# Kernel tuning notes

Measured on AMD Instinct MI355X. Metric: run time of the kernel, lower is better.

Reference implementation:

```python
import jax, jax.numpy as jnp
import numpy as np

N, E, G = 100000, 1600000, 64   # nodes, edges, graphs
IN, H, OUT = 32, 128, 3


def setup_inputs() -> dict:
    key = jax.random.key(0)
    ks = jax.random.split(key, 24)
    def w(k, i, o):
        return (jax.random.normal(k, (i, o), jnp.float32) / np.sqrt(i)).astype(jnp.float32)
    inp = {
        "x": jax.random.normal(ks[0], (N, IN), jnp.float32),
        "edge_index": jax.random.randint(ks[1], (2, E), 0, N, dtype=jnp.int32).astype(jnp.int64),
        "batch": jnp.sort(jax.random.randint(ks[2], (N,), 0, G, dtype=jnp.int32)).astype(jnp.int64),
        # SAGEConv layer 0 (in->hidden): lin_l (neighbors, with bias), lin_r (root, no bias)
        "Wl0": w(ks[3], IN, H), "bl0": jnp.zeros((H,), jnp.float32), "Wr0": w(ks[4], IN, H),
        # SAGEConv layers 1,2 (hidden->hidden)
        "Wl1": w(ks[5], H, H), "bl1": jnp.zeros((H,), jnp.float32), "Wr1": w(ks[6], H, H),
        "Wl2": w(ks[7], H, H), "bl2": jnp.zeros((H,), jnp.float32), "Wr2": w(ks[8], H, H),
        # output head
        "Wfc": w(ks[9], H, OUT), "bfc": jnp.zeros((OUT,), jnp.float32),
        # aux MLP on (dim1, dim3)
        "Wa1": w(ks[10], 2, H), "ba1": jnp.zeros((H,), jnp.float32),
        "Wa2": w(ks[11], H, H), "ba2": jnp.zeros((H,), jnp.float32),
        "Wao": w(ks[12], H, 1), "bao": jnp.zeros((1,), jnp.float32),
    }
    return inp


def _sage_conv(x, src, dst, Wl, bl, Wr):
    # PyG SAGEConv (mean aggr): out = lin_l(mean_{j in N(i)} x_j) + lin_r(x_i)
    msg = x[src]                                   # [E, d] gather
    agg = jax.ops.segment_sum(msg, dst, num_segments=N)
    cnt = jax.ops.segment_sum(jnp.ones((src.shape[0],), x.dtype), dst, num_segments=N)
    mean = agg / jnp.maximum(cnt, 1.0)[:, None]
    return mean @ Wl + bl + x @ Wr


def reference(x, edge_index, batch,
              Wl0, bl0, Wr0, Wl1, bl1, Wr1, Wl2, bl2, Wr2,
              Wfc, bfc, Wa1, ba1, Wa2, ba2, Wao, bao):
    src, dst = edge_index[0], edge_index[1]
    h = jax.nn.relu(_sage_conv(x, src, dst, Wl0, bl0, Wr0))   # dropout is identity in eval
    h = jax.nn.relu(_sage_conv(h, src, dst, Wl1, bl1, Wr1))
    h = jax.nn.relu(_sage_conv(h, src, dst, Wl2, bl2, Wr2))
    main = h @ Wfc + bfc                                      # [N, 3]
    dim1, dim3 = main[:, 0], main[:, 2]
    aux_in = jnp.stack([dim1, dim3], axis=-1)                 # [N, 2]
    a = jax.nn.relu(aux_in @ Wa1 + ba1)
    a = jax.nn.relu(a @ Wa2 + ba2)
    aux_out = (a @ Wao + bao)[:, 0]                           # [N]
    final = jnp.stack([dim1, aux_out, dim3], axis=-1)         # [N, 3]
    # global mean pool over graph ids
    s = jax.ops.segment_sum(final, batch, num_segments=G)
    c = jax.ops.segment_sum(jnp.ones((final.shape[0],), final.dtype), batch, num_segments=G)
    return s / jnp.maximum(c, 1.0)[:, None]                   # [G, 3]
```

## Files before the change

kernel.cpp:

```cpp
#include <hip/hip_runtime.h>

#define NR 128
#define PART_CH 4096
typedef unsigned short ushortT;
typedef __attribute__((ext_vector_type(8))) short short8;
typedef __attribute__((ext_vector_type(4))) float float4v;
typedef __attribute__((ext_vector_type(2))) float float2v;

__device__ __forceinline__ unsigned short f32_to_bf16_rne(float f) {
    unsigned u = __float_as_uint(f);
    unsigned r = (u + 0x7fffu + ((u >> 16) & 1u)) >> 16;
    return (unsigned short)r;
}

__device__ __forceinline__ unsigned char f32_to_fp8(float f) {
    return (unsigned char)(__builtin_amdgcn_cvt_pk_fp8_f32(f, f, 0, false) & 0xff);
}

__device__ __forceinline__ void accum8(float* acc, uint4 v) {
    unsigned u[4] = {v.x, v.y, v.z, v.w};
#pragma unroll
    for (int q = 0; q < 4; q++) {
        acc[2 * q]     += __uint_as_float(u[q] << 16);
        acc[2 * q + 1] += __uint_as_float(u[q] & 0xffff0000u);
    }
}


__launch_bounds__(256)
__global__ void bucket_count(const int* __restrict__ dst, int* __restrict__ bcnt, int E, int NB) {
    __shared__ int h[1024];
    int t = threadIdx.x;
    for (int j = t; j < NB; j += 256) h[j] = 0;
    __syncthreads();
    int e0 = blockIdx.x * PART_CH;
    int e1 = min(e0 + PART_CH, E);
    for (int base = e0; base < e1; base += 2048) {
        int idx = base + t;
        int d[8];
        int cnt = 0;
#pragma unroll
        for (int u = 0; u < 8; u++) {
            int e = idx + u * 256;
            if (e < e1) d[cnt++] = dst[e];
        }
        for (int u = 0; u < cnt; u++) atomicAdd(&h[d[u] >> 7], 1);
    }
    __syncthreads();
    for (int j = t; j < NB; j += 256) {
        int v = h[j];
        if (v) atomicAdd(&bcnt[j], v);
    }
}

__launch_bounds__(256)
__global__ void bucket_scan(const int* __restrict__ bcnt, int* __restrict__ bstart,
                            int* __restrict__ gcur, int NB, int E) {
    __shared__ int sh[256];
    int t = threadIdx.x;
    int v[4];
    int tot = 0;
#pragma unroll
    for (int j = 0; j < 4; j++) {
        int idx = t * 4 + j;
        v[j] = (idx < NB) ? bcnt[idx] : 0;
        tot += v[j];
    }
    sh[t] = tot;
    __syncthreads();
    for (int off = 1; off < 256; off <<= 1) {
        int add = (t >= off) ? sh[t - off] : 0;
        __syncthreads();
        sh[t] += add;
        __syncthreads();
    }
    int run = sh[t] - tot;
#pragma unroll
    for (int j = 0; j < 4; j++) {
        int idx = t * 4 + j;
        if (idx < NB) { bstart[idx] = run; gcur[idx] = run; }
        run += v[j];
    }
    if (t == 0) bstart[NB] = E;
}

__launch_bounds__(256)
__global__ void partition_edges(const int* __restrict__ src, const int* __restrict__ dst,
                                int* __restrict__ gcur, unsigned* __restrict__ packed,
                                int E, int NB) {
    __shared__ int hist[1024];
    __shared__ int base[1024];
    int t = threadIdx.x;
    int e0 = blockIdx.x * PART_CH;
    int e1 = min(e0 + PART_CH, E);
    for (int j = t; j < NB; j += 256) hist[j] = 0;
    __syncthreads();
    for (int bb = e0; bb < e1; bb += 2048) {
        int idx = bb + t;
        int d[8];
        int cnt = 0;
#pragma unroll
        for (int u = 0; u < 8; u++) {
            int e = idx + u * 256;
            if (e < e1) d[cnt++] = dst[e];
        }
        for (int u = 0; u < cnt; u++) atomicAdd(&hist[d[u] >> 7], 1);
    }
    __syncthreads();
    for (int j = t; j < NB; j += 256) {
        int h = hist[j];
        base[j] = h ? atomicAdd(&gcur[j], h) : 0;
    }
    __syncthreads();
    for (int j = t; j < NB; j += 256) hist[j] = base[j];
    __syncthreads();
    for (int bb = e0; bb < e1; bb += 2048) {
        int idx = bb + t;
        int d[8], s[8];
        int cnt = 0;
#pragma unroll
        for (int u = 0; u < 8; u++) {
            int e = idx + u * 256;
            if (e < e1) { d[cnt] = dst[e]; s[cnt] = src[e]; cnt++; }
        }
        for (int u = 0; u < cnt; u++) {
            int dd = d[u];
            int pos = atomicAdd(&hist[dd >> 7], 1);
            packed[pos] = (unsigned)s[u] | ((unsigned)(dd & (NR - 1)) << 17);
        }
    }
}

__launch_bounds__(256)
__global__ void bucket_sort(const unsigned* __restrict__ packed, const int* __restrict__ bstart,
                            int* __restrict__ row_start, int* __restrict__ srcs, int N) {
    __shared__ int cnt[NR];
    __shared__ int sc[NR];
    __shared__ int cur[NR];
    int b = blockIdx.x, t = threadIdx.x;
    int nb0 = b * NR;
    int nnode = min(NR, N - nb0);
    int lo = bstart[b], hi = bstart[b + 1];
    if (t < NR) cnt[t] = 0;
    __syncthreads();
    for (int bb = lo; bb < hi; bb += 2048) {
        int idx = bb + t;
        unsigned pk[8];
        int c = 0;
#pragma unroll
        for (int u = 0; u < 8; u++) {
            int e = idx + u * 256;
            if (e < hi) pk[c++] = packed[e];
        }
        for (int u = 0; u < c; u++) atomicAdd(&cnt[pk[u] >> 17], 1);
    }
    __syncthreads();
    if (t < NR) sc[t] = cnt[t];
    __syncthreads();
    for (int off = 1; off < NR; off <<= 1) {
        int add = (t >= off && t < NR) ? sc[t - off] : 0;
        __syncthreads();
        if (t < NR) sc[t] += add;
        __syncthreads();
    }
    if (t < nnode) {
        int s = lo + sc[t] - cnt[t];
        row_start[nb0 + t] = s;
        cur[t] = s;
    }
    if (t == 0 && nb0 + nnode == N) row_start[N] = hi;
    __syncthreads();
    for (int bb = lo; bb < hi; bb += 2048) {
        int idx = bb + t;
        unsigned pk[8];
        int c = 0;
#pragma unroll
        for (int u = 0; u < 8; u++) {
            int e = idx + u * 256;
            if (e < hi) pk[c++] = packed[e];
        }
        for (int u = 0; u < c; u++) {
            int pos = atomicAdd(&cur[pk[u] >> 17], 1);
            srcs[pos] = (int)(pk[u] & 0x1FFFFu);
        }
    }
}


__global__ void prep_fused(const float* __restrict__ x, ushortT* __restrict__ xbf, int n4,
                           const float* __restrict__ Wl0, const float* __restrict__ Wr0,
                           const float* __restrict__ Wl1, const float* __restrict__ Wr1,
                           const float* __restrict__ Wl2, const float* __restrict__ Wr2,
                           const float* __restrict__ Wa2,
                           ushortT* __restrict__ Wt0, ushortT* __restrict__ Wt1,
                           ushortT* __restrict__ Wt2, ushortT* __restrict__ Wa2t) {
    int tid0 = blockIdx.x * 256 + threadIdx.x;
    if (tid0 < n4) {
        float4 v = ((const float4*)x)[tid0];
        ushort4 o;
        o.x = f32_to_bf16_rne(v.x);
        o.y = f32_to_bf16_rne(v.y);
        o.z = f32_to_bf16_rne(v.z);
        o.w = f32_to_bf16_rne(v.w);
        ((ushort4*)xbf)[tid0] = o;
        return;
    }
    int tid = tid0 - n4;
    if (tid < 8192) {
        int col = tid >> 6, k = tid & 63;
        float v = (k < 32) ? Wl0[k * 128 + col] : Wr0[(k - 32) * 128 + col];
        Wt0[col * 64 + ((k + 8 * col) & 63)] = f32_to_bf16_rne(v);
    } else if (tid < 8192 + 32768) {
        int j = tid - 8192;
        int col = j >> 8, k = j & 255;
        float v = (k < 128) ? Wl1[k * 128 + col] : Wr1[(k - 128) * 128 + col];
        Wt1[col * 256 + ((k + 8 * col) & 255)] = f32_to_bf16_rne(v);
    } else if (tid < 8192 + 65536) {
        int j = tid - 8192 - 32768;
        int col = j >> 8, k = j & 255;
        float v = (k < 128) ? Wl2[k * 128 + col] : Wr2[(k - 128) * 128 + col];
        Wt2[col * 256 + ((k + 8 * col) & 255)] = f32_to_bf16_rne(v);
    } else if (tid < 8192 + 65536 + 16384) {
        int j = tid - 8192 - 65536;
        int col = j >> 7, k = j & 127;
        Wa2t[col * 128 + ((k + 8 * col) & 127)] = f32_to_bf16_rne(Wa2[k * 128 + col]);
    }
}


template <bool FP8, int NKS>
__device__ __forceinline__ void gather_accum(const void* __restrict__ gat, int s, int q, float* ag) {
    if constexpr (FP8) {
        const uint2* hp = (const uint2*)gat;
        size_t base = (size_t)s * 16 + q;
        uint2 c[NKS];
#pragma unroll
        for (int ks = 0; ks < NKS; ks++) c[ks] = hp[base + ks * 4];
#pragma unroll
        for (int ks = 0; ks < NKS; ks++) {
            float2v l0 = __builtin_amdgcn_cvt_pk_f32_fp8(c[ks].x, false);
            float2v h0 = __builtin_amdgcn_cvt_pk_f32_fp8(c[ks].x, true);
            float2v l1 = __builtin_amdgcn_cvt_pk_f32_fp8(c[ks].y, false);
            float2v h1 = __builtin_amdgcn_cvt_pk_f32_fp8(c[ks].y, true);
            ag[ks * 8 + 0] += l0.x; ag[ks * 8 + 1] += l0.y;
            ag[ks * 8 + 2] += h0.x; ag[ks * 8 + 3] += h0.y;
            ag[ks * 8 + 4] += l1.x; ag[ks * 8 + 5] += l1.y;
            ag[ks * 8 + 6] += h1.x; ag[ks * 8 + 7] += h1.y;
        }
    } else {
        const uint4* xp = (const uint4*)gat;
        uint4 v = xp[(size_t)s * 4 + q];
        accum8(ag, v);
    }
}

template <int KH, bool IN_FP8>
__launch_bounds__(256, 2)
__global__ void gemm_agg(const void* __restrict__ gat, const ushortT* __restrict__ Ah,
                         const int* __restrict__ srcs, const int* __restrict__ rs,
                         const ushortT* __restrict__ Wt, const float* __restrict__ bias,
                         ushortT* __restrict__ outbf, unsigned char* __restrict__ outf8, int n) {
    constexpr int KT = 2 * KH;
    constexpr int NKS = KH / 32;
    __shared__ __attribute__((aligned(16))) ushortT sW[128 * KT];
    int t = threadIdx.x;
    constexpr int TOT16 = 128 * KT * 2 / 16;
    {
        const uint4* Wg = (const uint4*)Wt;
        uint4* Ws = (uint4*)sW;
#pragma unroll
        for (int j = 0; j < TOT16 / 256; j++) Ws[t + j * 256] = Wg[t + j * 256];
    }
    int wv = t >> 6, lane = t & 63;
    int q = lane >> 4, cid = lane & 15;
    int rbase = blockIdx.x * 128 + wv * 32;
    int r0 = rbase + cid, r1 = r0 + 16;
    int r0c = min(r0, n - 1), r1c = min(r1, n - 1);

    float ag0[NKS * 8], ag1[NKS * 8];
#pragma unroll
    for (int j = 0; j < NKS * 8; j++) { ag0[j] = 0.f; ag1[j] = 0.f; }
    int lo0 = rs[r0c], n0 = rs[r0c + 1] - lo0;
    int lo1 = rs[r1c], n1 = rs[r1c + 1] - lo1;
    int mx = max(n0, n1);
    for (int i = 0; i < mx; i += 2) {
        bool v00 = i < n0, v01 = (i + 1) < n0;
        bool v10 = i < n1, v11 = (i + 1) < n1;
        int s00 = srcs[v00 ? lo0 + i : 0];
        int s01 = srcs[v01 ? lo0 + i + 1 : 0];
        int s10 = srcs[v10 ? lo1 + i : 0];
        int s11 = srcs[v11 ? lo1 + i + 1 : 0];
        if (v00) gather_accum<IN_FP8, NKS>(gat, s00, q, ag0);
        if (v01) gather_accum<IN_FP8, NKS>(gat, s01, q, ag0);
        if (v10) gather_accum<IN_FP8, NKS>(gat, s10, q, ag1);
        if (v11) gather_accum<IN_FP8, NKS>(gat, s11, q, ag1);
    }
    float inv0 = 1.0f / (float)max(n0, 1);
    float inv1 = 1.0f / (float)max(n1, 1);
    short8 am0[NKS], am1[NKS];
#pragma unroll
    for (int ks = 0; ks < NKS; ks++)
#pragma unroll
        for (int j = 0; j < 8; j++) {
            am0[ks][j] = (short)f32_to_bf16_rne(ag0[ks * 8 + j] * inv0);
            am1[ks][j] = (short)f32_to_bf16_rne(ag1[ks * 8 + j] * inv1);
        }
    __syncthreads();

    float4v acc[2][8];
#pragma unroll
    for (int i = 0; i < 2; i++)
#pragma unroll
        for (int j = 0; j < 8; j++) acc[i][j] = (float4v){0.f, 0.f, 0.f, 0.f};
    int swz = q * 8 + 8 * cid;
#pragma unroll
    for (int ks = 0; ks < KT / 32; ++ks) {
        int kk = ks * 32;
        short8 a0, a1;
        if (ks < NKS) {
            a0 = am0[ks];
            a1 = am1[ks];
        } else {
            int kc = kk - KH;
            a0 = *(const short8*)(Ah + (size_t)r0c * KH + kc + q * 8);
            a1 = *(const short8*)(Ah + (size_t)r1c * KH + kc + q * 8);
        }
#pragma unroll
        for (int j = 0; j < 8; ++j) {
            int col = j * 16 + cid;
            int p = (kk + swz + j * 128) & (KT - 1);
            short8 b = *(const short8*)(sW + col * KT + p);
            acc[0][j] = __builtin_amdgcn_mfma_f32_16x16x32_bf16(a0, b, acc[0][j], 0, 0, 0);
            acc[1][j] = __builtin_amdgcn_mfma_f32_16x16x32_bf16(a1, b, acc[1][j], 0, 0, 0);
        }
    }
    float bo[8];
#pragma unroll
    for (int j = 0; j < 8; ++j) bo[j] = bias[j * 16 + cid];
#pragma unroll
    for (int i = 0; i < 2; ++i) {
#pragma unroll
        for (int rr = 0; rr < 4; ++rr) {
            int row = rbase + i * 16 + q * 4 + rr;
            if (row < n) {
#pragma unroll
                for (int j = 0; j < 8; ++j) {
                    int col = j * 16 + cid;
                    float v = fmaxf(acc[i][j][rr] + bo[j], 0.f);
                    outbf[(size_t)row * 128 + col] = f32_to_bf16_rne(v);
                    outf8[(size_t)row * 128 + col] = f32_to_fp8(v);
                }
            }
        }
    }
}


__launch_bounds__(256, 2)
__global__ void gemm_agg_fin(const void* __restrict__ gat, const ushortT* __restrict__ Ah,
                             const int* __restrict__ srcs, const int* __restrict__ rs,
                             const ushortT* __restrict__ Wt, const float* __restrict__ bias,
                             const float* __restrict__ Wfc, const float* __restrict__ bfc,
                             const ushortT* __restrict__ Wa2t, const float* __restrict__ Wa1,
                             const float* __restrict__ ba1, const float* __restrict__ ba2,
                             const float* __restrict__ Wao, const float* __restrict__ bao,
                             float* __restrict__ fin, int n) {
    constexpr int KH = 128, KT = 256, NKS = 4;
    __shared__ __attribute__((aligned(16))) ushortT sW[128 * KT];
    __shared__ float sD1[128], sD3[128];
    __shared__ float sWa1a[128], sWa1b[128], sBa1[128];
    int t = threadIdx.x;
    {
        const uint4* Wg = (const uint4*)Wt;
        uint4* Ws = (uint4*)sW;
#pragma unroll
        for (int j = 0; j < 16; j++) Ws[t + j * 256] = Wg[t + j * 256];
    }
    if (t < 128) { sWa1a[t] = Wa1[t]; sWa1b[t] = Wa1[128 + t]; sBa1[t] = ba1[t]; }
    int wv = t >> 6, lane = t & 63;
    int q = lane >> 4, cid = lane & 15;
    int blk0 = blockIdx.x * 128;
    int rbase = blk0 + wv * 32;
    int r0 = rbase + cid, r1 = r0 + 16;
    int r0c = min(r0, n - 1), r1c = min(r1, n - 1);

    float ag0[NKS * 8], ag1[NKS * 8];
#pragma unroll
    for (int j = 0; j < NKS * 8; j++) { ag0[j] = 0.f; ag1[j] = 0.f; }
    int lo0 = rs[r0c], n0 = rs[r0c + 1] - lo0;
    int lo1 = rs[r1c], n1 = rs[r1c + 1] - lo1;
    int mx = max(n0, n1);
    for (int i = 0; i < mx; i += 2) {
        bool v00 = i < n0, v01 = (i + 1) < n0;
        bool v10 = i < n1, v11 = (i + 1) < n1;
        int s00 = srcs[v00 ? lo0 + i : 0];
        int s01 = srcs[v01 ? lo0 + i + 1 : 0];
        int s10 = srcs[v10 ? lo1 + i : 0];
        int s11 = srcs[v11 ? lo1 + i + 1 : 0];
        if (v00) gather_accum<true, NKS>(gat, s00, q, ag0);
        if (v01) gather_accum<true, NKS>(gat, s01, q, ag0);
        if (v10) gather_accum<true, NKS>(gat, s10, q, ag1);
        if (v11) gather_accum<true, NKS>(gat, s11, q, ag1);
    }
    float inv0 = 1.0f / (float)max(n0, 1);
    float inv1 = 1.0f / (float)max(n1, 1);
    short8 am0[NKS], am1[NKS];
#pragma unroll
    for (int ks = 0; ks < NKS; ks++)
#pragma unroll
        for (int j = 0; j < 8; j++) {
            am0[ks][j] = (short)f32_to_bf16_rne(ag0[ks * 8 + j] * inv0);
            am1[ks][j] = (short)f32_to_bf16_rne(ag1[ks * 8 + j] * inv1);
        }
    __syncthreads();

    float4v acc[2][8];
#pragma unroll
    for (int i = 0; i < 2; i++)
#pragma unroll
        for (int j = 0; j < 8; j++) acc[i][j] = (float4v){0.f, 0.f, 0.f, 0.f};
    int swz = q * 8 + 8 * cid;
#pragma unroll
    for (int ks = 0; ks < KT / 32; ++ks) {
        int kk = ks * 32;
        short8 a0, a1;
        if (ks < NKS) {
            a0 = am0[ks];
            a1 = am1[ks];
        } else {
            int kc = kk - KH;
            a0 = *(const short8*)(Ah + (size_t)r0c * KH + kc + q * 8);
            a1 = *(const short8*)(Ah + (size_t)r1c * KH + kc + q * 8);
        }
#pragma unroll
        for (int j = 0; j < 8; ++j) {
            int col = j * 16 + cid;
            int p = (kk + swz + j * 128) & (KT - 1);
            short8 b = *(const short8*)(sW + col * KT + p);
            acc[0][j] = __builtin_amdgcn_mfma_f32_16x16x32_bf16(a0, b, acc[0][j], 0, 0, 0);
            acc[1][j] = __builtin_amdgcn_mfma_f32_16x16x32_bf16(a1, b, acc[1][j], 0, 0, 0);
        }
    }

    float bo[8], w1[8], w3[8];
#pragma unroll
    for (int j = 0; j < 8; ++j) {
        int col = j * 16 + cid;
        bo[j] = bias[col];
        w1[j] = Wfc[col * 3 + 0];
        w3[j] = Wfc[col * 3 + 2];
    }
    float bfc0 = bfc[0], bfc2 = bfc[2];
#pragma unroll
    for (int i = 0; i < 2; ++i) {
#pragma unroll
        for (int rr = 0; rr < 4; ++rr) {
            float p1 = 0.f, p3 = 0.f;
#pragma unroll
            for (int j = 0; j < 8; ++j) {
                float v = fmaxf(acc[i][j][rr] + bo[j], 0.f);
                p1 += v * w1[j];
                p3 += v * w3[j];
            }
            p1 += __shfl_xor(p1, 1, 64); p3 += __shfl_xor(p3, 1, 64);
            p1 += __shfl_xor(p1, 2, 64); p3 += __shfl_xor(p3, 2, 64);
            p1 += __shfl_xor(p1, 4, 64); p3 += __shfl_xor(p3, 4, 64);
            p1 += __shfl_xor(p1, 8, 64); p3 += __shfl_xor(p3, 8, 64);
            int rowl = wv * 32 + i * 16 + q * 4 + rr;
            if (cid == 0) {
                float d1 = p1 + bfc0, d3 = p3 + bfc2;
                sD1[rowl] = d1;
                sD3[rowl] = d3;
                int row = blk0 + rowl;
                if (row < n) {
                    fin[(size_t)row * 3 + 0] = d1;
                    fin[(size_t)row * 3 + 2] = d3;
                }
            }
        }
    }
    __syncthreads();

    {
        const uint4* Wg = (const uint4*)Wa2t;
        uint4* Ws = (uint4*)sW;
#pragma unroll
        for (int j = 0; j < 8; j++) Ws[t + j * 256] = Wg[t + j * 256];
    }
    __syncthreads();

    int rl0 = wv * 32 + cid, rl1 = rl0 + 16;
    float d1a = sD1[rl0], d3a = sD3[rl0];
    float d1b = sD1[rl1], d3b = sD3[rl1];
    float4v hacc[2][8];
#pragma unroll
    for (int i = 0; i < 2; i++)
#pragma unroll
        for (int j = 0; j < 8; j++) hacc[i][j] = (float4v){0.f, 0.f, 0.f, 0.f};
#pragma unroll
    for (int ks = 0; ks < 4; ++ks) {
        int k0 = ks * 32 + q * 8;
        short8 a0, a1;
#pragma unroll
        for (int j = 0; j < 8; ++j) {
            int k = k0 + j;
            float w0 = sWa1a[k], w1h = sWa1b[k], bb = sBa1[k];
            float v0 = fmaxf(fmaf(d1a, w0, fmaf(d3a, w1h, bb)), 0.f);
            float v1 = fmaxf(fmaf(d1b, w0, fmaf(d3b, w1h, bb)), 0.f);
            a0[j] = (short)f32_to_bf16_rne(v0);
            a1[j] = (short)f32_to_bf16_rne(v1);
        }
        int p = (ks * 32 + swz) & 127;
#pragma unroll
        for (int j = 0; j < 8; ++j) {
            short8 b = *(const short8*)(sW + (j * 16 + cid) * 128 + p);
            hacc[0][j] = __builtin_amdgcn_mfma_f32_16x16x32_bf16(a0, b, hacc[0][j], 0, 0, 0);
            hacc[1][j] = __builtin_amdgcn_mfma_f32_16x16x32_bf16(a1, b, hacc[1][j], 0, 0, 0);
        }
    }
    float b2[8], wo[8];
#pragma unroll
    for (int j = 0; j < 8; ++j) {
        int col = j * 16 + cid;
        b2[j] = ba2[col];
        wo[j] = Wao[col];
    }
    float bao0 = bao[0];
#pragma unroll
    for (int i = 0; i < 2; ++i) {
#pragma unroll
        for (int rr = 0; rr < 4; ++rr) {
            float s = 0.f;
#pragma unroll
            for (int j = 0; j < 8; ++j) s += fmaxf(hacc[i][j][rr] + b2[j], 0.f) * wo[j];
            s += __shfl_xor(s, 1, 64);
            s += __shfl_xor(s, 2, 64);
            s += __shfl_xor(s, 4, 64);
            s += __shfl_xor(s, 8, 64);
            int row = blk0 + wv * 32 + i * 16 + q * 4 + rr;
            if (cid == 0 && row < n) fin[(size_t)row * 3 + 1] = s + bao0;
        }
    }
}


__global__ void pool_kernel(const float* __restrict__ fin, const int* __restrict__ batch,
                            float* __restrict__ out, int n) {
    int g = blockIdx.x, t = threadIdx.x;
    int lo = 0, hi = n;
    while (lo < hi) { int mid = (lo + hi) >> 1; if (batch[mid] < g) lo = mid + 1; else hi = mid; }
    int start = lo;
    lo = 0; hi = n;
    while (lo < hi) { int mid = (lo + hi) >> 1; if (batch[mid] < g + 1) lo = mid + 1; else hi = mid; }
    int end = lo;
    float s0 = 0.f, s1 = 0.f, s2 = 0.f;
    for (int i = start + t; i < end; i += 256) {
        s0 += fin[(size_t)i * 3 + 0];
        s1 += fin[(size_t)i * 3 + 1];
        s2 += fin[(size_t)i * 3 + 2];
    }
    __shared__ float r0[256], r1[256], r2[256];
    r0[t] = s0; r1[t] = s1; r2[t] = s2;
    __syncthreads();
    for (int off = 128; off > 0; off >>= 1) {
        if (t < off) { r0[t] += r0[t + off]; r1[t] += r1[t + off]; r2[t] += r2[t + off]; }
        __syncthreads();
    }
    if (t == 0) {
        float c = (float)max(end - start, 1);
        out[g * 3 + 0] = r0[0] / c;
        out[g * 3 + 1] = r1[0] / c;
        out[g * 3 + 2] = r2[0] / c;
    }
}


extern "C" void kernel_launch(void* const* d_in, const int* in_sizes, int n_in,
                              void* d_out, int out_size, void* d_ws, size_t ws_size,
                              hipStream_t stream) {
    const float* x    = (const float*)d_in[0];
    const int*   ei   = (const int*)d_in[1];
    const int*   batch= (const int*)d_in[2];
    const float* Wl0  = (const float*)d_in[3];
    const float* bl0  = (const float*)d_in[4];
    const float* Wr0  = (const float*)d_in[5];
    const float* Wl1  = (const float*)d_in[6];
    const float* bl1  = (const float*)d_in[7];
    const float* Wr1  = (const float*)d_in[8];
    const float* Wl2  = (const float*)d_in[9];
    const float* bl2  = (const float*)d_in[10];
    const float* Wr2  = (const float*)d_in[11];
    const float* Wfc  = (const float*)d_in[12];
    const float* bfc  = (const float*)d_in[13];
    const float* Wa1  = (const float*)d_in[14];
    const float* ba1  = (const float*)d_in[15];
    const float* Wa2  = (const float*)d_in[16];
    const float* ba2  = (const float*)d_in[17];
    const float* Wao  = (const float*)d_in[18];
    const float* bao  = (const float*)d_in[19];

    const int N = in_sizes[0] / 32;
    const int E = in_sizes[1] / 2;
    const int G = out_size / 3;
    const int* src = ei;
    const int* dst = ei + E;
    float* out = (float*)d_out;
    const int NB = (N + NR - 1) / NR;

    char* p = (char*)d_ws;
    auto carve = [&](size_t bytes) {
        void* r = (void*)p;
        p += (bytes + 255) & ~(size_t)255;
        return r;
    };
    int*           bcnt     = (int*)carve((size_t)NB * 4);
    int*           bstart   = (int*)carve((size_t)(NB + 1) * 4);
    int*           gcur     = (int*)carve((size_t)NB * 4);
    int*           row_start= (int*)carve((size_t)(N + 1) * 4);
    unsigned*      packed   = (unsigned*)carve((size_t)E * 4);
    int*           srcs     = (int*)carve((size_t)E * 4);
    ushortT*       xbf      = (ushortT*)carve((size_t)N * 32 * 2);
    ushortT*       hbf0     = (ushortT*)carve((size_t)N * 128 * 2);
    ushortT*       hbf1     = (ushortT*)carve((size_t)N * 128 * 2);
    unsigned char* hf8_0    = (unsigned char*)carve((size_t)N * 128);
    unsigned char* hf8_1    = (unsigned char*)carve((size_t)N * 128);
    float*         fin      = (float*)carve((size_t)N * 3 * 4);
    ushortT*       Wt0      = (ushortT*)carve((size_t)128 * 64 * 2);
    ushortT*       Wt1      = (ushortT*)carve((size_t)128 * 256 * 2);
    ushortT*       Wt2      = (ushortT*)carve((size_t)128 * 256 * 2);
    ushortT*       Wa2t     = (ushortT*)carve((size_t)128 * 128 * 2);

    const int gemm_grid = (N + 127) / 128;
    const int part_grid = (E + PART_CH - 1) / PART_CH;
    const int n4 = N * 32 / 4;

    prep_fused<<<(n4 + 90112 + 255) / 256, 256, 0, stream>>>(
        x, xbf, n4, Wl0, Wr0, Wl1, Wr1, Wl2, Wr2, Wa2, Wt0, Wt1, Wt2, Wa2t);

    hipMemsetAsync(bcnt, 0, (size_t)NB * 4, stream);
    bucket_count<<<part_grid, 256, 0, stream>>>(dst, bcnt, E, NB);
    bucket_scan<<<1, 256, 0, stream>>>(bcnt, bstart, gcur, NB, E);
    partition_edges<<<part_grid, 256, 0, stream>>>(src, dst, gcur, packed, E, NB);
    bucket_sort<<<NB, 256, 0, stream>>>(packed, bstart, row_start, srcs, N);

    gemm_agg<32, false><<<gemm_grid, 256, 0, stream>>>(
        (const void*)xbf, xbf, srcs, row_start, Wt0, bl0, hbf0, hf8_0, N);
    gemm_agg<128, true><<<gemm_grid, 256, 0, stream>>>(
        (const void*)hf8_0, hbf0, srcs, row_start, Wt1, bl1, hbf1, hf8_1, N);
    gemm_agg_fin<<<gemm_grid, 256, 0, stream>>>(
        (const void*)hf8_1, hbf1, srcs, row_start, Wt2, bl2, Wfc, bfc,
        Wa2t, Wa1, ba1, ba2, Wao, bao, fin, N);

    pool_kernel<<<G, 256, 0, stream>>>(fin, batch, out, N);
}
```

Baseline: 408.9 us.

## Shrink GEMM-agg tiles to 64 rows, halve LDS weights, batch 8-edge gathers

The fused aggregate+GEMM kernels now handle 16 rows per wave (64 per block) instead of 32. The weight matrix is split into two 128-wide halves loaded into LDS one after the other, which halves the shared-memory footprint, and launch bounds rise from 2 to 4 blocks per CU. The neighbor gather is restructured to prefetch 8 source indices and issue 8 feature loads at once, using 32-byte FP8 loads per lane, with the FP8 output columns permuted to match. The goal is more memory-level parallelism and occupancy for the latency-bound gathers, at the cost of reloading weights per block, an extra sync, and more blocks.

```diff
diff --git a/kernel.cpp b/kernel.cpp
--- a/kernel.cpp
+++ b/kernel.cpp
@@ -23,6 +23,19 @@
     for (int q = 0; q < 4; q++) {
         acc[2 * q]     += __uint_as_float(u[q] << 16);
         acc[2 * q + 1] += __uint_as_float(u[q] & 0xffff0000u);
+    }
+}
+
+__device__ __forceinline__ void accum32_fp8(float* ag, uint4 A, uint4 B) {
+    unsigned w[8] = {A.x, A.y, A.z, A.w, B.x, B.y, B.z, B.w};
+#pragma unroll
+    for (int m = 0; m < 8; m++) {
+        float2v lo = __builtin_amdgcn_cvt_pk_f32_fp8(w[m], false);
+        float2v hi = __builtin_amdgcn_cvt_pk_f32_fp8(w[m], true);
+        ag[4 * m + 0] += lo.x;
+        ag[4 * m + 1] += lo.y;
+        ag[4 * m + 2] += hi.x;
+        ag[4 * m + 3] += hi.y;
     }
 }
 
@@ -214,12 +227,12 @@
         int j = tid - 8192;
         int col = j >> 8, k = j & 255;
         float v = (k < 128) ? Wl1[k * 128 + col] : Wr1[(k - 128) * 128 + col];
-        Wt1[col * 256 + ((k + 8 * col) & 255)] = f32_to_bf16_rne(v);
+        Wt1[(k >> 7) * 16384 + col * 128 + (((k & 127) + 8 * col) & 127)] = f32_to_bf16_rne(v);
     } else if (tid < 8192 + 65536) {
         int j = tid - 8192 - 32768;
         int col = j >> 8, k = j & 255;
         float v = (k < 128) ? Wl2[k * 128 + col] : Wr2[(k - 128) * 128 + col];
-        Wt2[col * 256 + ((k + 8 * col) & 255)] = f32_to_bf16_rne(v);
+        Wt2[(k >> 7) * 16384 + col * 128 + (((k & 127) + 8 * col) & 127)] = f32_to_bf16_rne(v);
     } else if (tid < 8192 + 65536 + 16384) {
         int j = tid - 8192 - 65536;
         int col = j >> 7, k = j & 127;
@@ -228,135 +241,160 @@
 }
 
 
-template <bool FP8, int NKS>
-__device__ __forceinline__ void gather_accum(const void* __restrict__ gat, int s, int q, float* ag) {
-    if constexpr (FP8) {
-        const uint2* hp = (const uint2*)gat;
-        size_t base = (size_t)s * 16 + q;
-        uint2 c[NKS];
-#pragma unroll
-        for (int ks = 0; ks < NKS; ks++) c[ks] = hp[base + ks * 4];
-#pragma unroll
-        for (int ks = 0; ks < NKS; ks++) {
-            float2v l0 = __builtin_amdgcn_cvt_pk_f32_fp8(c[ks].x, false);
-            float2v h0 = __builtin_amdgcn_cvt_pk_f32_fp8(c[ks].x, true);
-            float2v l1 = __builtin_amdgcn_cvt_pk_f32_fp8(c[ks].y, false);
-            float2v h1 = __builtin_amdgcn_cvt_pk_f32_fp8(c[ks].y, true);
-            ag[ks * 8 + 0] += l0.x; ag[ks * 8 + 1] += l0.y;
-            ag[ks * 8 + 2] += h0.x; ag[ks * 8 + 3] += h0.y;
-            ag[ks * 8 + 4] += l1.x; ag[ks * 8 + 5] += l1.y;
-            ag[ks * 8 + 6] += h1.x; ag[ks * 8 + 7] += h1.y;
-        }
-    } else {
-        const uint4* xp = (const uint4*)gat;
-        uint4 v = xp[(size_t)s * 4 + q];
-        accum8(ag, v);
-    }
-}
+__device__ __forceinline__ void gather_fp8(const uint4* __restrict__ hp, const int* __restrict__ srcs,
+                                           int lo, int deg, int q, float* ag) {
+    int nb = (deg + 7) >> 3;
+    if (nb == 0) return;
+    int last = lo + deg - 1;
+    int sA[8];
+#pragma unroll
+    for (int u = 0; u < 8; u++) sA[u] = srcs[min(lo + u, last)];
+    for (int b = 0; b < nb; b++) {
+        uint4 va[8], vb[8];
+#pragma unroll
+        for (int u = 0; u < 8; u++) {
+            size_t bs = (size_t)sA[u] * 8 + q * 2;
+            va[u] = hp[bs];
+            vb[u] = hp[bs + 1];
+        }
+        int e0 = lo + (b + 1) * 8;
+        if (b + 1 < nb) {
+#pragma unroll
+            for (int u = 0; u < 8; u++) sA[u] = srcs[min(e0 + u, last)];
+        }
+        int rem = deg - b * 8;
+#pragma unroll
+        for (int u = 0; u < 8; u++)
+            if (u < rem) accum32_fp8(ag, va[u], vb[u]);
+    }
+}
+
+__device__ __forceinline__ void gather_bf16(const uint4* __restrict__ xp, const int* __restrict__ srcs,
+                                            int lo, int deg, int q, float* ag) {
+    int nb = (deg + 7) >> 3;
+    if (nb == 0) return;
+    int last = lo + deg - 1;
+    int sA[8];
+#pragma unroll
+    for (int u = 0; u < 8; u++) sA[u] = srcs[min(lo + u, last)];
+    for (int b = 0; b < nb; b++) {
+        uint4 va[8];
+#pragma unroll
+        for (int u = 0; u < 8; u++) va[u] = xp[(size_t)sA[u] * 4 + q];
+        int e0 = lo + (b + 1) * 8;
+        if (b + 1 < nb) {
+#pragma unroll
+            for (int u = 0; u < 8; u++) sA[u] = srcs[min(e0 + u, last)];
+        }
+        int rem = deg - b * 8;
+#pragma unroll
+        for (int u = 0; u < 8; u++)
+            if (u < rem) accum8(ag, va[u]);
+    }
+}
+
 
 template <int KH, bool IN_FP8>
-__launch_bounds__(256, 2)
+__launch_bounds__(256, 4)
 __global__ void gemm_agg(const void* __restrict__ gat, const ushortT* __restrict__ Ah,
                          const int* __restrict__ srcs, const int* __restrict__ rs,
                          const ushortT* __restrict__ Wt, const float* __restrict__ bias,
                          ushortT* __restrict__ outbf, unsigned char* __restrict__ outf8, int n) {
-    constexpr int KT = 2 * KH;
     constexpr int NKS = KH / 32;
-    __shared__ __attribute__((aligned(16))) ushortT sW[128 * KT];
+    constexpr int KTH = (KH == 32) ? 64 : 128;
+    __shared__ __attribute__((aligned(16))) ushortT sW[128 * KTH];
     int t = threadIdx.x;
-    constexpr int TOT16 = 128 * KT * 2 / 16;
     {
         const uint4* Wg = (const uint4*)Wt;
         uint4* Ws = (uint4*)sW;
 #pragma unroll
-        for (int j = 0; j < TOT16 / 256; j++) Ws[t + j * 256] = Wg[t + j * 256];
+        for (int j = 0; j < (128 * KTH / 8) / 256; j++) Ws[t + j * 256] = Wg[t + j * 256];
     }
     int wv = t >> 6, lane = t & 63;
     int q = lane >> 4, cid = lane & 15;
-    int rbase = blockIdx.x * 128 + wv * 32;
-    int r0 = rbase + cid, r1 = r0 + 16;
-    int r0c = min(r0, n - 1), r1c = min(r1, n - 1);
-
-    float ag0[NKS * 8], ag1[NKS * 8];
-#pragma unroll
-    for (int j = 0; j < NKS * 8; j++) { ag0[j] = 0.f; ag1[j] = 0.f; }
-    int lo0 = rs[r0c], n0 = rs[r0c + 1] - lo0;
-    int lo1 = rs[r1c], n1 = rs[r1c + 1] - lo1;
-    int mx = max(n0, n1);
-    for (int i = 0; i < mx; i += 2) {
-        bool v00 = i < n0, v01 = (i + 1) < n0;
-        bool v10 = i < n1, v11 = (i + 1) < n1;
-        int s00 = srcs[v00 ? lo0 + i : 0];
-        int s01 = srcs[v01 ? lo0 + i + 1 : 0];
-        int s10 = srcs[v10 ? lo1 + i : 0];
-        int s11 = srcs[v11 ? lo1 + i + 1 : 0];
-        if (v00) gather_accum<IN_FP8, NKS>(gat, s00, q, ag0);
-        if (v01) gather_accum<IN_FP8, NKS>(gat, s01, q, ag0);
-        if (v10) gather_accum<IN_FP8, NKS>(gat, s10, q, ag1);
-        if (v11) gather_accum<IN_FP8, NKS>(gat, s11, q, ag1);
-    }
-    float inv0 = 1.0f / (float)max(n0, 1);
-    float inv1 = 1.0f / (float)max(n1, 1);
-    short8 am0[NKS], am1[NKS];
+    int row = blockIdx.x * 64 + wv * 16 + cid;
+    int rc = min(row, n - 1);
+
+    float ag[NKS * 8];
+#pragma unroll
+    for (int j = 0; j < NKS * 8; j++) ag[j] = 0.f;
+    int lo = rs[rc], deg = rs[rc + 1] - lo;
+    if constexpr (IN_FP8) gather_fp8((const uint4*)gat, srcs, lo, deg, q, ag);
+    else                  gather_bf16((const uint4*)gat, srcs, lo, deg, q, ag);
+    float inv = 1.0f / (float)max(deg, 1);
+    short8 am[NKS];
 #pragma unroll
     for (int ks = 0; ks < NKS; ks++)
 #pragma unroll
-        for (int j = 0; j < 8; j++) {
-            am0[ks][j] = (short)f32_to_bf16_rne(ag0[ks * 8 + j] * inv0);
-            am1[ks][j] = (short)f32_to_bf16_rne(ag1[ks * 8 + j] * inv1);
-        }
-    __syncthreads();
-
-    float4v acc[2][8];
-#pragma unroll
-    for (int i = 0; i < 2; i++)
-#pragma unroll
-        for (int j = 0; j < 8; j++) acc[i][j] = (float4v){0.f, 0.f, 0.f, 0.f};
-    int swz = q * 8 + 8 * cid;
-#pragma unroll
-    for (int ks = 0; ks < KT / 32; ++ks) {
-        int kk = ks * 32;
-        short8 a0, a1;
-        if (ks < NKS) {
-            a0 = am0[ks];
-            a1 = am1[ks];
-        } else {
-            int kc = kk - KH;
-            a0 = *(const short8*)(Ah + (size_t)r0c * KH + kc + q * 8);
-            a1 = *(const short8*)(Ah + (size_t)r1c * KH + kc + q * 8);
-        }
+        for (int j = 0; j < 8; j++) am[ks][j] = (short)f32_to_bf16_rne(ag[ks * 8 + j] * inv);
+    __syncthreads();
+
+    float4v acc[8];
+#pragma unroll
+    for (int j = 0; j < 8; j++) acc[j] = (float4v){0.f, 0.f, 0.f, 0.f};
+    int pbase = q * 8 + 8 * cid;
+#pragma unroll
+    for (int ks = 0; ks < NKS; ks++) {
+        int p = (ks * 32 + pbase) & (KTH - 1);
 #pragma unroll
         for (int j = 0; j < 8; ++j) {
-            int col = j * 16 + cid;
-            int p = (kk + swz + j * 128) & (KT - 1);
-            short8 b = *(const short8*)(sW + col * KT + p);
-            acc[0][j] = __builtin_amdgcn_mfma_f32_16x16x32_bf16(a0, b, acc[0][j], 0, 0, 0);
-            acc[1][j] = __builtin_amdgcn_mfma_f32_16x16x32_bf16(a1, b, acc[1][j], 0, 0, 0);
+            short8 b = *(const short8*)(sW + (j * 16 + cid) * KTH + p);
+            acc[j] = __builtin_amdgcn_mfma_f32_16x16x32_bf16(am[ks], b, acc[j], 0, 0, 0);
+        }
+    }
+    if constexpr (KH == 32) {
+        short8 ah = *(const short8*)(Ah + (size_t)rc * 32 + q * 8);
+        int p = (32 + pbase) & 63;
+#pragma unroll
+        for (int j = 0; j < 8; ++j) {
+            short8 b = *(const short8*)(sW + (j * 16 + cid) * 64 + p);
+            acc[j] = __builtin_amdgcn_mfma_f32_16x16x32_bf16(ah, b, acc[j], 0, 0, 0);
+        }
+    } else {
+        short8 ah[4];
+#pragma unroll
+        for (int ks = 0; ks < 4; ks++)
+            ah[ks] = *(const short8*)(Ah + (size_t)rc * 128 + ks * 32 + q * 8);
+        __syncthreads();
+        {
+            const uint4* Wg = (const uint4*)(Wt + 128 * 128);
+            uint4* Ws = (uint4*)sW;
+#pragma unroll
+            for (int j = 0; j < 8; j++) Ws[t + j * 256] = Wg[t + j * 256];
+        }
+        __syncthreads();
+#pragma unroll
+        for (int ks = 0; ks < 4; ks++) {
+            int p = (ks * 32 + pbase) & 127;
+#pragma unroll
+            for (int j = 0; j < 8; ++j) {
+                short8 b = *(const short8*)(sW + (j * 16 + cid) * 128 + p);
+                acc[j] = __builtin_amdgcn_mfma_f32_16x16x32_bf16(ah[ks], b, acc[j], 0, 0, 0);
+            }
         }
     }
     float bo[8];
 #pragma unroll
     for (int j = 0; j < 8; ++j) bo[j] = bias[j * 16 + cid];
-#pragma unroll
-    for (int i = 0; i < 2; ++i) {
-#pragma unroll
-        for (int rr = 0; rr < 4; ++rr) {
-            int row = rbase + i * 16 + q * 4 + rr;
-            if (row < n) {
-#pragma unroll
-                for (int j = 0; j < 8; ++j) {
-                    int col = j * 16 + cid;
-                    float v = fmaxf(acc[i][j][rr] + bo[j], 0.f);
-                    outbf[(size_t)row * 128 + col] = f32_to_bf16_rne(v);
-                    outf8[(size_t)row * 128 + col] = f32_to_fp8(v);
-                }
+    int orow = blockIdx.x * 64 + wv * 16 + q * 4;
+#pragma unroll
+    for (int rr = 0; rr < 4; ++rr) {
+        int r = orow + rr;
+        if (r < n) {
+#pragma unroll
+            for (int j = 0; j < 8; ++j) {
+                int col = j * 16 + cid;
+                float v = fmaxf(acc[j][rr] + bo[j], 0.f);
+                outbf[(size_t)r * 128 + col] = f32_to_bf16_rne(v);
+                int pc = ((col >> 3) & 3) * 32 + ((col >> 5) << 3) + (col & 7);
+                outf8[(size_t)r * 128 + pc] = f32_to_fp8(v);
             }
         }
     }
 }
 
 
-__launch_bounds__(256, 2)
+__launch_bounds__(256, 4)
 __global__ void gemm_agg_fin(const void* __restrict__ gat, const ushortT* __restrict__ Ah,
                              const int* __restrict__ srcs, const int* __restrict__ rs,
                              const ushortT* __restrict__ Wt, const float* __restrict__ bias,
@@ -365,80 +403,67 @@
                              const float* __restrict__ ba1, const float* __restrict__ ba2,
                              const float* __restrict__ Wao, const float* __restrict__ bao,
                              float* __restrict__ fin, int n) {
-    constexpr int KH = 128, KT = 256, NKS = 4;
-    __shared__ __attribute__((aligned(16))) ushortT sW[128 * KT];
-    __shared__ float sD1[128], sD3[128];
+    __shared__ __attribute__((aligned(16))) ushortT sW[128 * 128];
+    __shared__ float sD1[64], sD3[64];
     __shared__ float sWa1a[128], sWa1b[128], sBa1[128];
     int t = threadIdx.x;
     {
         const uint4* Wg = (const uint4*)Wt;
         uint4* Ws = (uint4*)sW;
 #pragma unroll
-        for (int j = 0; j < 16; j++) Ws[t + j * 256] = Wg[t + j * 256];
+        for (int j = 0; j < 8; j++) Ws[t + j * 256] = Wg[t + j * 256];
     }
     if (t < 128) { sWa1a[t] = Wa1[t]; sWa1b[t] = Wa1[128 + t]; sBa1[t] = ba1[t]; }
     int wv = t >> 6, lane = t & 63;
     int q = lane >> 4, cid = lane & 15;
-    int blk0 = blockIdx.x * 128;
-    int rbase = blk0 + wv * 32;
-    int r0 = rbase + cid, r1 = r0 + 16;
-    int r0c = min(r0, n - 1), r1c = min(r1, n - 1);
-
-    float ag0[NKS * 8], ag1[NKS * 8];
-#pragma unroll
-    for (int j = 0; j < NKS * 8; j++) { ag0[j] = 0.f; ag1[j] = 0.f; }
-    int lo0 = rs[r0c], n0 = rs[r0c + 1] - lo0;
-    int lo1 = rs[r1c], n1 = rs[r1c + 1] - lo1;
-    int mx = max(n0, n1);
-    for (int i = 0; i < mx; i += 2) {
-        bool v00 = i < n0, v01 = (i + 1) < n0;
-        bool v10 = i < n1, v11 = (i + 1) < n1;
-        int s00 = srcs[v00 ? lo0 + i : 0];
-        int s01 = srcs[v01 ? lo0 + i + 1 : 0];
-        int s10 = srcs[v10 ? lo1 + i : 0];
-        int s11 = srcs[v11 ? lo1 + i + 1 : 0];
-        if (v00) gather_accum<true, NKS>(gat, s00, q, ag0);
-        if (v01) gather_accum<true, NKS>(gat, s01, q, ag0);
-        if (v10) gather_accum<true, NKS>(gat, s10, q, ag1);
-        if (v11) gather_accum<true, NKS>(gat, s11, q, ag1);
-    }
-    float inv0 = 1.0f / (float)max(n0, 1);
-    float inv1 = 1.0f / (float)max(n1, 1);
-    short8 am0[NKS], am1[NKS];
-#pragma unroll
-    for (int ks = 0; ks < NKS; ks++)
-#pragma unroll
-        for (int j = 0; j < 8; j++) {
-            am0[ks][j] = (short)f32_to_bf16_rne(ag0[ks * 8 + j] * inv0);
-            am1[ks][j] = (short)f32_to_bf16_rne(ag1[ks * 8 + j] * inv1);
-        }
-    __syncthreads();
-
-    float4v acc[2][8];
-#pragma unroll
-    for (int i = 0; i < 2; i++)
-#pragma unroll
-        for (int j = 0; j < 8; j++) acc[i][j] = (float4v){0.f, 0.f, 0.f, 0.f};
-    int swz = q * 8 + 8 * cid;
-#pragma unroll
-    for (int ks = 0; ks < KT / 32; ++ks) {
-        int kk = ks * 32;
-        short8 a0, a1;
-        if (ks < NKS) {
-            a0 = am0[ks];
-            a1 = am1[ks];
-        } else {
-            int kc = kk - KH;
-            a0 = *(const short8*)(Ah + (size_t)r0c * KH + kc + q * 8);
-            a1 = *(const short8*)(Ah + (size_t)r1c * KH + kc + q * 8);
-        }
+    int row = blockIdx.x * 64 + wv * 16 + cid;
+    int rc = min(row, n - 1);
+
+    float ag[32];
+#pragma unroll
+    for (int j = 0; j < 32; j++) ag[j] = 0.f;
+    int lo = rs[rc], deg = rs[rc + 1] - lo;
+    gather_fp8((const uint4*)gat, srcs, lo, deg, q, ag);
+    float inv = 1.0f / (float)max(deg, 1);
+    short8 am[4];
+#pragma unroll
+    for (int ks = 0; ks < 4; ks++)
+#pragma unroll
+        for (int j = 0; j < 8; j++) am[ks][j] = (short)f32_to_bf16_rne(ag[ks * 8 + j] * inv);
+    __syncthreads();
+
+    float4v acc[8];
+#pragma unroll
+    for (int j = 0; j < 8; j++) acc[j] = (float4v){0.f, 0.f, 0.f, 0.f};
+    int pbase = q * 8 + 8 * cid;
+#pragma unroll
+    for (int ks = 0; ks < 4; ks++) {
+        int p = (ks * 32 + pbase) & 127;
 #pragma unroll
         for (int j = 0; j < 8; ++j) {
-            int col = j * 16 + cid;
-            int p = (kk + swz + j * 128) & (KT - 1);
-            short8 b = *(const short8*)(sW + col * KT + p);
-            acc[0][j] = __builtin_amdgcn_mfma_f32_16x16x32_bf16(a0, b, acc[0][j], 0, 0, 0);
-            acc[1][j] = __builtin_amdgcn_mfma_f32_16x16x32_bf16(a1, b, acc[1][j], 0, 0, 0);
+            short8 b = *(const short8*)(sW + (j * 16 + cid) * 128 + p);
+            acc[j] = __builtin_amdgcn_mfma_f32_16x16x32_bf16(am[ks], b, acc[j], 0, 0, 0);
+        }
+    }
+    short8 ah[4];
+#pragma unroll
+    for (int ks = 0; ks < 4; ks++)
+        ah[ks] = *(const short8*)(Ah + (size_t)rc * 128 + ks * 32 + q * 8);
+    __syncthreads();
+    {
+        const uint4* Wg = (const uint4*)(Wt + 128 * 128);
+        uint4* Ws = (uint4*)sW;
+#pragma unroll
+        for (int j = 0; j < 8; j++) Ws[t + j * 256] = Wg[t + j * 256];
+    }
+    __syncthreads();
+#pragma unroll
+    for (int ks = 0; ks < 4; ks++) {
+        int p = (ks * 32 + pbase) & 127;
+#pragma unroll
+        for (int j = 0; j < 8; ++j) {
+            short8 b = *(const short8*)(sW + (j * 16 + cid) * 128 + p);
+            acc[j] = __builtin_amdgcn_mfma_f32_16x16x32_bf16(ah[ks], b, acc[j], 0, 0, 0);
         }
     }
 
@@ -452,35 +477,31 @@
     }
     float bfc0 = bfc[0], bfc2 = bfc[2];
 #pragma unroll
-    for (int i = 0; i < 2; ++i) {
-#pragma unroll
-        for (int rr = 0; rr < 4; ++rr) {
-            float p1 = 0.f, p3 = 0.f;
-#pragma unroll
-            for (int j = 0; j < 8; ++j) {
-                float v = fmaxf(acc[i][j][rr] + bo[j], 0.f);
-                p1 += v * w1[j];
-                p3 += v * w3[j];
+    for (int rr = 0; rr < 4; ++rr) {
+        float p1 = 0.f, p3 = 0.f;
+#pragma unroll
+        for (int j = 0; j < 8; ++j) {
+            float v = fmaxf(acc[j][rr] + bo[j], 0.f);
+            p1 += v * w1[j];
+            p3 += v * w3[j];
+        }
+        p1 += __shfl_xor(p1, 1, 64); p3 += __shfl_xor(p3, 1, 64);
+        p1 += __shfl_xor(p1, 2, 64); p3 += __shfl_xor(p3, 2, 64);
+        p1 += __shfl_xor(p1, 4, 64); p3 += __shfl_xor(p3, 4, 64);
+        p1 += __shfl_xor(p1, 8, 64); p3 += __shfl_xor(p3, 8, 64);
+        if (cid == 0) {
+            int rowl = wv * 16 + q * 4 + rr;
+            float d1 = p1 + bfc0, d3 = p3 + bfc2;
+            sD1[rowl] = d1;
+            sD3[rowl] = d3;
+            int r = blockIdx.x * 64 + rowl;
+            if (r < n) {
+                fin[(size_t)r * 3 + 0] = d1;
+                fin[(size_t)r * 3 + 2] = d3;
             }
-            p1 += __shfl_xor(p1, 1, 64); p3 += __shfl_xor(p3, 1, 64);
-            p1 += __shfl_xor(p1, 2, 64); p3 += __shfl_xor(p3, 2, 64);
-            p1 += __shfl_xor(p1, 4, 64); p3 += __shfl_xor(p3, 4, 64);
-            p1 += __shfl_xor(p1, 8, 64); p3 += __shfl_xor(p3, 8, 64);
-            int rowl = wv * 32 + i * 16 + q * 4 + rr;
-            if (cid == 0) {
-                float d1 = p1 + bfc0, d3 = p3 + bfc2;
-                sD1[rowl] = d1;
-                sD3[rowl] = d3;
-                int row = blk0 + rowl;
-                if (row < n) {
-                    fin[(size_t)row * 3 + 0] = d1;
-                    fin[(size_t)row * 3 + 2] = d3;
-                }
-            }
-        }
-    }
-    __syncthreads();
-
+        }
+    }
+    __syncthreads();
     {
         const uint4* Wg = (const uint4*)Wa2t;
         uint4* Ws = (uint4*)sW;
@@ -489,33 +510,26 @@
     }
     __syncthreads();
 
-    int rl0 = wv * 32 + cid, rl1 = rl0 + 16;
-    float d1a = sD1[rl0], d3a = sD3[rl0];
-    float d1b = sD1[rl1], d3b = sD3[rl1];
-    float4v hacc[2][8];
-#pragma unroll
-    for (int i = 0; i < 2; i++)
-#pragma unroll
-        for (int j = 0; j < 8; j++) hacc[i][j] = (float4v){0.f, 0.f, 0.f, 0.f};
+    int rl = wv * 16 + cid;
+    float d1a = sD1[rl], d3a = sD3[rl];
+    float4v hacc[8];
+#pragma unroll
+    for (int j = 0; j < 8; j++) hacc[j] = (float4v){0.f, 0.f, 0.f, 0.f};
 #pragma unroll
     for (int ks = 0; ks < 4; ++ks) {
         int k0 = ks * 32 + q * 8;
-        short8 a0, a1;
+        short8 a0;
 #pragma unroll
         for (int j = 0; j < 8; ++j) {
             int k = k0 + j;
-            float w0 = sWa1a[k], w1h = sWa1b[k], bb = sBa1[k];
-            float v0 = fmaxf(fmaf(d1a, w0, fmaf(d3a, w1h, bb)), 0.f);
-            float v1 = fmaxf(fmaf(d1b, w0, fmaf(d3b, w1h, bb)), 0.f);
+            float v0 = fmaxf(fmaf(d1a, sWa1a[k], fmaf(d3a, sWa1b[k], sBa1[k])), 0.f);
             a0[j] = (short)f32_to_bf16_rne(v0);
-            a1[j] = (short)f32_to_bf16_rne(v1);
-        }
-        int p = (ks * 32 + swz) & 127;
+        }
+        int p = (ks * 32 + pbase) & 127;
 #pragma unroll
         for (int j = 0; j < 8; ++j) {
             short8 b = *(const short8*)(sW + (j * 16 + cid) * 128 + p);
-            hacc[0][j] = __builtin_amdgcn_mfma_f32_16x16x32_bf16(a0, b, hacc[0][j], 0, 0, 0);
-            hacc[1][j] = __builtin_amdgcn_mfma_f32_16x16x32_bf16(a1, b, hacc[1][j], 0, 0, 0);
+            hacc[j] = __builtin_amdgcn_mfma_f32_16x16x32_bf16(a0, b, hacc[j], 0, 0, 0);
         }
     }
     float b2[8], wo[8];
@@ -527,19 +541,16 @@
     }
     float bao0 = bao[0];
 #pragma unroll
-    for (int i = 0; i < 2; ++i) {
-#pragma unroll
-        for (int rr = 0; rr < 4; ++rr) {
-            float s = 0.f;
-#pragma unroll
-            for (int j = 0; j < 8; ++j) s += fmaxf(hacc[i][j][rr] + b2[j], 0.f) * wo[j];
-            s += __shfl_xor(s, 1, 64);
-            s += __shfl_xor(s, 2, 64);
-            s += __shfl_xor(s, 4, 64);
-            s += __shfl_xor(s, 8, 64);
-            int row = blk0 + wv * 32 + i * 16 + q * 4 + rr;
-            if (cid == 0 && row < n) fin[(size_t)row * 3 + 1] = s + bao0;
-        }
+    for (int rr = 0; rr < 4; ++rr) {
+        float s = 0.f;
+#pragma unroll
+        for (int j = 0; j < 8; ++j) s += fmaxf(hacc[j][rr] + b2[j], 0.f) * wo[j];
+        s += __shfl_xor(s, 1, 64);
+        s += __shfl_xor(s, 2, 64);
+        s += __shfl_xor(s, 4, 64);
+        s += __shfl_xor(s, 8, 64);
+        int r = blockIdx.x * 64 + wv * 16 + q * 4 + rr;
+        if (cid == 0 && r < n) fin[(size_t)r * 3 + 1] = s + bao0;
     }
 }
 
@@ -630,7 +641,7 @@
     ushortT*       Wt2      = (ushortT*)carve((size_t)128 * 256 * 2);
     ushortT*       Wa2t     = (ushortT*)carve((size_t)128 * 128 * 2);
 
-    const int gemm_grid = (N + 127) / 128;
+    const int gemm_grid = (N + 63) / 64;
     const int part_grid = (E + PART_CH - 1) / PART_CH;
     const int n4 = N * 32 / 4;
 
```

After: 368.5 us. 9.9% less time.
